# Kernel tuning notes

Hardware: AMD Instinct MI355X
Metric: run time of the kernel (lower is better)

## Reference

```python
import jax, jax.numpy as jnp
import numpy as np

N_COMS = 8
THRESHOLD = 1.0


def setup_inputs() -> dict:
    key = jax.random.key(0)
    k1, k2 = jax.random.split(key)
    N, D, F = 100000, 256, 256
    x = jax.random.normal(k1, (N, F), dtype=jnp.float32)
    z = jax.random.normal(k2, (N, D), dtype=jnp.float32)
    return {"x": x, "z": z}


def reference(x, z):
    N, D = z.shape
    C = N_COMS
    # phi[:, i] = mean of i-th equal chunk of z along features (tensor_split with D % C == 0)
    phi = z.reshape(N, C, D // C).mean(axis=-1)            # [N, C]
    phi = jax.nn.softmax(phi, axis=0)                      # column-wise softmax over nodes

    # chunk_computer, algebraically identical to the masked NxCxCxN einsum:
    # m_1[n,c] = phi[n,c] * sum_{l>n} r[l];  m_2[n,c] = phi[n,c] * sum_{i<n} r[i]
    # => node_weight = phi * (sum(r) - r)[:, None], with r = rowsum(phi)
    r = phi.sum(axis=1)                                    # [N]
    node_weight = phi * (r.sum() - r)[:, None]             # [N, C]

    max_value = node_weight.max(axis=1, keepdims=True)     # [N, 1]
    node_mask = (node_weight == max_value) | (node_weight >= THRESHOLD)  # [N, C] bool

    # x_commun_list: per community, x zeroed outside masked nodes -> stacked [C, N, F]
    x_parts = jnp.where(node_mask.T[:, :, None], x[None, :, :], jnp.zeros((), x.dtype))
    return x_parts, node_mask
```

## Files before the change

### kernel.cpp

```cpp
#include <hip/hip_runtime.h>
#include <cstdint>
#include <cmath>

#define NN 100000
#define NC 8
#define NF 256
#define XPARTS_FLOATS ((size_t)NC * NN * NF)

typedef float f32x4 __attribute__((ext_vector_type(4)));

__global__ __launch_bounds__(256) void k_phi_raw(const f32x4* __restrict__ z4,
                                                 double* __restrict__ raw) {
    int gid = blockIdx.x * 256 + threadIdx.x;
    int n = gid >> 6;
    int l = gid & 63;
    if (n >= NN) return;
    f32x4 v = z4[(size_t)n * 64 + l];
    double s = ((double)v.x + (double)v.y) + ((double)v.z + (double)v.w);
    s += __shfl_xor(s, 1, 64);
    s += __shfl_xor(s, 2, 64);
    s += __shfl_xor(s, 4, 64);
    if ((l & 7) == 0) raw[(size_t)n * NC + (l >> 3)] = s * (1.0 / 32.0);
}

__global__ __launch_bounds__(256) void k_col_partial(const double* __restrict__ raw,
                                                     double* __restrict__ part) {
    __shared__ double ss[256][NC];
    int tid = threadIdx.x;
    int gtid = blockIdx.x * 256 + tid;
    double s[NC];
#pragma unroll
    for (int c = 0; c < NC; ++c) s[c] = 0.0;
    for (int n = gtid; n < NN; n += 256 * 256) {
        const double* rp = raw + (size_t)n * NC;
#pragma unroll
        for (int c = 0; c < NC; ++c) s[c] += exp(rp[c]);
    }
#pragma unroll
    for (int c = 0; c < NC; ++c) ss[tid][c] = s[c];
    __syncthreads();
    for (int off = 128; off > 0; off >>= 1) {
        if (tid < off) {
#pragma unroll
            for (int c = 0; c < NC; ++c) ss[tid][c] += ss[tid + off][c];
        }
        __syncthreads();
    }
    if (tid == 0) {
#pragma unroll
        for (int c = 0; c < NC; ++c) part[(size_t)blockIdx.x * NC + c] = ss[0][c];
    }
}

__global__ __launch_bounds__(256) void k_col_final(const double* __restrict__ part,
                                                   double* __restrict__ fin) {
    __shared__ double ss[256][NC];
    int tid = threadIdx.x;
#pragma unroll
    for (int c = 0; c < NC; ++c) ss[tid][c] = part[(size_t)tid * NC + c];
    __syncthreads();
    for (int off = 128; off > 0; off >>= 1) {
        if (tid < off) {
#pragma unroll
            for (int c = 0; c < NC; ++c) ss[tid][c] += ss[tid + off][c];
        }
        __syncthreads();
    }
    if (tid == 0) {
#pragma unroll
        for (int c = 0; c < NC; ++c) fin[c] = ss[0][c];
    }
}

__global__ __launch_bounds__(256) void k_mask(const double* __restrict__ raw,
                                              const double* __restrict__ fin,
                                              float* __restrict__ mask_out) {
    int n = blockIdx.x * blockDim.x + threadIdx.x;
    if (n >= NN) return;
    double phi[NC];
    double r = 0.0;
#pragma unroll
    for (int c = 0; c < NC; ++c) {
        phi[c] = exp(raw[(size_t)n * NC + c]) / fin[c];
        r += phi[c];
    }
    double f = 8.0 - r;
    double w[NC];
    double wmax = -1e300;
#pragma unroll
    for (int c = 0; c < NC; ++c) { w[c] = phi[c] * f; wmax = fmax(wmax, w[c]); }
#pragma unroll
    for (int c = 0; c < NC; ++c) {
        bool bit = (w[c] == wmax) || (w[c] >= 1.0);
        mask_out[(size_t)n * NC + c] = bit ? 1.0f : 0.0f;
    }
}

__global__ __launch_bounds__(256) void k_scatter(const f32x4* __restrict__ x4,
                                                 const float* __restrict__ mask,
                                                 f32x4* __restrict__ out4) {
    __shared__ float mlds[64 * NC];
    int tid = threadIdx.x;
    int b = blockIdx.x;
    int r0 = b * 64;
    int nrows = NN - r0; if (nrows > 64) nrows = 64;
    int nvec = nrows * 64;
    size_t base = (size_t)r0 * 64;

    for (int k = tid; k < nrows * NC; k += 256)
        mlds[k] = mask[(size_t)r0 * NC + k];

    f32x4 v[16];
#pragma unroll
    for (int i = 0; i < 16; ++i) {
        int idx = i * 256 + tid;
        v[i] = (idx < nvec) ? x4[base + idx] : (f32x4)(0.f);
    }
    __syncthreads();

    const f32x4 zz = (f32x4)(0.f);
#pragma unroll
    for (int c = 0; c < NC; ++c) {
        size_t cbase = (size_t)c * NN * 64 + base;
#pragma unroll
        for (int i = 0; i < 16; ++i) {
            int idx = i * 256 + tid;
            if (idx < nvec) {
                int lr = idx >> 6;
                bool bit = mlds[lr * NC + c] != 0.0f;
                __builtin_nontemporal_store(bit ? v[i] : zz, &out4[cbase + idx]);
            }
        }
    }
}

extern "C" void kernel_launch(void* const* d_in, const int* in_sizes, int n_in,
                              void* d_out, int out_size, void* d_ws, size_t ws_size,
                              hipStream_t stream) {
    const float* x = (const float*)d_in[0];
    const float* z = (const float*)d_in[1];
    float* out = (float*)d_out;

    double* raw  = (double*)out;
    double* part = (double*)(out + 2000000);
    double* fin  = (double*)(out + 2200000);
    float* mask_out = out + XPARTS_FLOATS;

    k_phi_raw    <<<(NN * 64 + 255) / 256, 256, 0, stream>>>((const f32x4*)z, raw);
    k_col_partial<<<256, 256, 0, stream>>>(raw, part);
    k_col_final  <<<1, 256, 0, stream>>>(part, fin);
    k_mask       <<<(NN + 255) / 256, 256, 0, stream>>>(raw, fin, mask_out);
    k_scatter    <<<(NN + 63) / 64, 256, 0, stream>>>((const f32x4*)x, mask_out, (f32x4*)out);
}
```

Before: 201.9 us.

## Fuse column-sum finalize and mask computation into scatter kernel using workspace

When the workspace is large enough, the intermediate raw and partial arrays move from the output buffer into the workspace. The final column reduction and the per-row mask computation are folded into the scatter kernel, which removes two kernel launches and the global mask round-trip. Each scatter block now redundantly reduces the 256 partial sums in shared memory, adding a small per-block prologue before the large write phase.

```diff
diff --git a/kernel.cpp b/kernel.cpp
--- a/kernel.cpp
+++ b/kernel.cpp
@@ -52,6 +52,75 @@
     }
 }
 
+__global__ __launch_bounds__(256) void k_scatter_fused(
+    const f32x4* __restrict__ x4, const double* __restrict__ raw,
+    const double* __restrict__ part, float* __restrict__ mask_out,
+    f32x4* __restrict__ out4) {
+    __shared__ double ss[256][NC];
+    __shared__ float mlds[64 * NC];
+    int tid = threadIdx.x;
+
+#pragma unroll
+    for (int c = 0; c < NC; ++c) ss[tid][c] = part[(size_t)tid * NC + c];
+    __syncthreads();
+    for (int off = 128; off > 0; off >>= 1) {
+        if (tid < off) {
+#pragma unroll
+            for (int c = 0; c < NC; ++c) ss[tid][c] += ss[tid + off][c];
+        }
+        __syncthreads();
+    }
+
+    int r0 = blockIdx.x * 64;
+    int nrows = NN - r0; if (nrows > 64) nrows = 64;
+
+    if (tid < nrows) {
+        int n = r0 + tid;
+        double phi[NC];
+        double r = 0.0;
+#pragma unroll
+        for (int c = 0; c < NC; ++c) {
+            phi[c] = exp(raw[(size_t)n * NC + c]) / ss[0][c];
+            r += phi[c];
+        }
+        double f = 8.0 - r;
+        double w[NC];
+        double wmax = -1e300;
+#pragma unroll
+        for (int c = 0; c < NC; ++c) { w[c] = phi[c] * f; wmax = fmax(wmax, w[c]); }
+#pragma unroll
+        for (int c = 0; c < NC; ++c) {
+            float bitf = ((w[c] == wmax) || (w[c] >= 1.0)) ? 1.0f : 0.0f;
+            mlds[tid * NC + c] = bitf;
+            mask_out[(size_t)n * NC + c] = bitf;
+        }
+    }
+    __syncthreads();
+
+    int nvec = nrows * 64;
+    size_t base = (size_t)r0 * 64;
+    f32x4 v[16];
+#pragma unroll
+    for (int i = 0; i < 16; ++i) {
+        int idx = i * 256 + tid;
+        v[i] = (idx < nvec) ? x4[base + idx] : (f32x4)(0.f);
+    }
+    const f32x4 zz = (f32x4)(0.f);
+#pragma unroll
+    for (int c = 0; c < NC; ++c) {
+        size_t cbase = (size_t)c * NN * 64 + base;
+#pragma unroll
+        for (int i = 0; i < 16; ++i) {
+            int idx = i * 256 + tid;
+            if (idx < nvec) {
+                int lr = idx >> 6;
+                bool bit = mlds[lr * NC + c] != 0.0f;
+                __builtin_nontemporal_store(bit ? v[i] : zz, &out4[cbase + idx]);
+            }
+        }
+    }
+}
+
 __global__ __launch_bounds__(256) void k_col_final(const double* __restrict__ part,
                                                    double* __restrict__ fin) {
     __shared__ double ss[256][NC];
@@ -101,15 +170,12 @@
                                                  f32x4* __restrict__ out4) {
     __shared__ float mlds[64 * NC];
     int tid = threadIdx.x;
-    int b = blockIdx.x;
-    int r0 = b * 64;
+    int r0 = blockIdx.x * 64;
     int nrows = NN - r0; if (nrows > 64) nrows = 64;
     int nvec = nrows * 64;
     size_t base = (size_t)r0 * 64;
-
     for (int k = tid; k < nrows * NC; k += 256)
         mlds[k] = mask[(size_t)r0 * NC + k];
-
     f32x4 v[16];
 #pragma unroll
     for (int i = 0; i < 16; ++i) {
@@ -117,7 +183,6 @@
         v[i] = (idx < nvec) ? x4[base + idx] : (f32x4)(0.f);
     }
     __syncthreads();
-
     const f32x4 zz = (f32x4)(0.f);
 #pragma unroll
     for (int c = 0; c < NC; ++c) {
@@ -137,18 +202,29 @@
 extern "C" void kernel_launch(void* const* d_in, const int* in_sizes, int n_in,
                               void* d_out, int out_size, void* d_ws, size_t ws_size,
                               hipStream_t stream) {
-    const float* x = (const float*)d_in[0];
-    const float* z = (const float*)d_in[1];
+    const f32x4* x4 = (const f32x4*)d_in[0];
+    const f32x4* z4 = (const f32x4*)d_in[1];
     float* out = (float*)d_out;
-
-    double* raw  = (double*)out;
-    double* part = (double*)(out + 2000000);
-    double* fin  = (double*)(out + 2200000);
     float* mask_out = out + XPARTS_FLOATS;
 
-    k_phi_raw    <<<(NN * 64 + 255) / 256, 256, 0, stream>>>((const f32x4*)z, raw);
-    k_col_partial<<<256, 256, 0, stream>>>(raw, part);
-    k_col_final  <<<1, 256, 0, stream>>>(part, fin);
-    k_mask       <<<(NN + 255) / 256, 256, 0, stream>>>(raw, fin, mask_out);
-    k_scatter    <<<(NN + 63) / 64, 256, 0, stream>>>((const f32x4*)x, mask_out, (f32x4*)out);
-}
+    const size_t RAW_BYTES  = (size_t)NN * NC * sizeof(double);
+    const size_t PART_BYTES = 256 * NC * sizeof(double);
+
+    if (ws_size >= RAW_BYTES + PART_BYTES) {
+        double* raw  = (double*)d_ws;
+        double* part = (double*)((char*)d_ws + RAW_BYTES);
+        k_phi_raw      <<<(NN * 64 + 255) / 256, 256, 0, stream>>>(z4, raw);
+        k_col_partial  <<<256, 256, 0, stream>>>(raw, part);
+        k_scatter_fused<<<(NN + 63) / 64, 256, 0, stream>>>(x4, raw, part,
+                                                            mask_out, (f32x4*)out);
+    } else {
+        double* raw  = (double*)out;
+        double* part = (double*)(out + 2000000);
+        double* fin  = (double*)(out + 2200000);
+        k_phi_raw    <<<(NN * 64 + 255) / 256, 256, 0, stream>>>(z4, raw);
+        k_col_partial<<<256, 256, 0, stream>>>(raw, part);
+        k_col_final  <<<1, 256, 0, stream>>>(part, fin);
+        k_mask       <<<(NN + 255) / 256, 256, 0, stream>>>(raw, fin, mask_out);
+        k_scatter    <<<(NN + 63) / 64, 256, 0, stream>>>(x4, mask_out, (f32x4*)out);
+    }
+}
```

Result: no change. 200.2 us (-0.8%).

## Split scatter into per-community blocks and move scratch buffers to workspace

Applied to the files above, without the earlier changes.

The scatter kernel now launches one block per (32-row chunk, community) pair, so each block reads x once and writes a contiguous slice of a single output plane. The old version had each block load 64 rows into registers and write all 8 planes. This trades register pressure and scattered multi-plane writes for 8x more reads of x, which should mostly hit L2/MALL. The intermediate raw/part/fin buffers also move into the workspace when it is large enough, instead of aliasing the output.

```diff
diff --git a/kernel.cpp b/kernel.cpp
--- a/kernel.cpp
+++ b/kernel.cpp
@@ -6,6 +6,9 @@
 #define NC 8
 #define NF 256
 #define XPARTS_FLOATS ((size_t)NC * NN * NF)
+#define PLANE_VEC ((size_t)NN * 64)
+#define CHUNK_ROWS 32
+#define NCHUNK (NN / CHUNK_ROWS)
 
 typedef float f32x4 __attribute__((ext_vector_type(4)));
 
@@ -96,59 +99,55 @@
     }
 }
 
-__global__ __launch_bounds__(256) void k_scatter(const f32x4* __restrict__ x4,
-                                                 const float* __restrict__ mask,
-                                                 f32x4* __restrict__ out4) {
-    __shared__ float mlds[64 * NC];
+__global__ __launch_bounds__(256) void k_scatter_lin(
+    const f32x4* __restrict__ x4, const float* __restrict__ mask,
+    f32x4* __restrict__ out4) {
+    int bid = blockIdx.x;
+    int c = bid & 7;
+    int chunk = bid >> 3;
+    int r0 = chunk * CHUNK_ROWS;
+    size_t base = (size_t)r0 * 64;
+    __shared__ float bits[CHUNK_ROWS];
     int tid = threadIdx.x;
-    int b = blockIdx.x;
-    int r0 = b * 64;
-    int nrows = NN - r0; if (nrows > 64) nrows = 64;
-    int nvec = nrows * 64;
-    size_t base = (size_t)r0 * 64;
-
-    for (int k = tid; k < nrows * NC; k += 256)
-        mlds[k] = mask[(size_t)r0 * NC + k];
-
-    f32x4 v[16];
+    if (tid < CHUNK_ROWS) bits[tid] = mask[(size_t)(r0 + tid) * NC + c];
+    __syncthreads();
+    const f32x4 zz = (f32x4)(0.f);
+    size_t obase = (size_t)c * PLANE_VEC + base;
 #pragma unroll
-    for (int i = 0; i < 16; ++i) {
+    for (int i = 0; i < 8; ++i) {
         int idx = i * 256 + tid;
-        v[i] = (idx < nvec) ? x4[base + idx] : (f32x4)(0.f);
-    }
-    __syncthreads();
-
-    const f32x4 zz = (f32x4)(0.f);
-#pragma unroll
-    for (int c = 0; c < NC; ++c) {
-        size_t cbase = (size_t)c * NN * 64 + base;
-#pragma unroll
-        for (int i = 0; i < 16; ++i) {
-            int idx = i * 256 + tid;
-            if (idx < nvec) {
-                int lr = idx >> 6;
-                bool bit = mlds[lr * NC + c] != 0.0f;
-                __builtin_nontemporal_store(bit ? v[i] : zz, &out4[cbase + idx]);
-            }
-        }
+        f32x4 v = x4[base + idx];
+        bool bit = bits[idx >> 6] != 0.0f;
+        __builtin_nontemporal_store(bit ? v : zz, &out4[obase + idx]);
     }
 }
 
 extern "C" void kernel_launch(void* const* d_in, const int* in_sizes, int n_in,
                               void* d_out, int out_size, void* d_ws, size_t ws_size,
                               hipStream_t stream) {
-    const float* x = (const float*)d_in[0];
-    const float* z = (const float*)d_in[1];
+    const f32x4* x4 = (const f32x4*)d_in[0];
+    const f32x4* z4 = (const f32x4*)d_in[1];
     float* out = (float*)d_out;
-
-    double* raw  = (double*)out;
-    double* part = (double*)(out + 2000000);
-    double* fin  = (double*)(out + 2200000);
     float* mask_out = out + XPARTS_FLOATS;
 
-    k_phi_raw    <<<(NN * 64 + 255) / 256, 256, 0, stream>>>((const f32x4*)z, raw);
+    const size_t RAW_BYTES  = (size_t)NN * NC * sizeof(double);
+    const size_t PART_BYTES = 256 * NC * sizeof(double);
+    const size_t FIN_BYTES  = NC * sizeof(double);
+
+    double *raw, *part, *fin;
+    if (ws_size >= RAW_BYTES + PART_BYTES + FIN_BYTES) {
+        raw  = (double*)d_ws;
+        part = (double*)((char*)d_ws + RAW_BYTES);
+        fin  = (double*)((char*)d_ws + RAW_BYTES + PART_BYTES);
+    } else {
+        raw  = (double*)out;
+        part = (double*)(out + 2000000);
+        fin  = (double*)(out + 2200000);
+    }
+
+    k_phi_raw    <<<(NN * 64 + 255) / 256, 256, 0, stream>>>(z4, raw);
     k_col_partial<<<256, 256, 0, stream>>>(raw, part);
     k_col_final  <<<1, 256, 0, stream>>>(part, fin);
     k_mask       <<<(NN + 255) / 256, 256, 0, stream>>>(raw, fin, mask_out);
-    k_scatter    <<<(NN + 63) / 64, 256, 0, stream>>>((const f32x4*)x, mask_out, (f32x4*)out);
+    k_scatter_lin<<<NCHUNK * NC, 256, 0, stream>>>(x4, mask_out, (f32x4*)out);
 }
```

After: 223.7 us. 10.8% more time.
